# Optimization experiments

Measured on AMD Instinct MI355X. Metric: run time of the kernel, lower is better.

Reference implementation:

```python
import jax, jax.numpy as jnp
import numpy as np

EPS = 1e-6
DECAY = 0.9   # spike_decay
THR = 0.5     # spike_threshold
SBETA = 10.0  # surrogate beta
KW = 4        # depthwise short-conv kernel width (causal)


def _rms(x, w):
    return x * jax.lax.rsqrt(jnp.mean(x * x, axis=-1, keepdims=True) + EPS) * w


def setup_inputs() -> dict:
    B, T, D, H, dk, dv, r, dff = 2, 2048, 1024, 8, 64, 64, 64, 4096
    keys = iter(jax.random.split(jax.random.key(0), 24))
    def g(shape, s=0.02):
        return jax.random.normal(next(keys), shape, jnp.float32) * s
    return {
        'x': jax.random.normal(next(keys), (B, T, D), jnp.float32),
        'norm_in_w': jnp.ones((D,), jnp.float32),
        'conv_w': g((D, 1, KW), 0.3),
        'conv_b': jnp.zeros((D,), jnp.float32),
        'Wq': g((D, H * dk)),
        'Wk': g((D, H * dk)),
        'Wv': g((D, H * dv)),
        'Wo': g((H * dv, D)),
        'Wspike': g((D, H * dk), 0.1),  # larger init so LIF actually spikes
        'Wau': g((D, r)),
        'bau': jnp.zeros((r,), jnp.float32),
        'Wad': g((r, H * dk)),
        'bad': jnp.zeros((H * dk,), jnp.float32),
        'alpha_spike': jnp.zeros((1, H, dk), jnp.float32),
        'Wbeta': g((D, H)),
        'bbeta': jnp.zeros((H,), jnp.float32),
        'beta_spike': jnp.zeros((1, H, dk), jnp.float32),
        'head_norm_w': jnp.ones((H, dv), jnp.float32),
        'Wu1': g((D, r)),
        'bu1': jnp.zeros((r,), jnp.float32),
        'Wu2': g((r, D)),
        'bu2': jnp.zeros((D,), jnp.float32),
        'ff_norm_w': jnp.ones((D,), jnp.float32),
        'Wff1': g((D, dff)),
        'Wff3': g((D, dff)),
        'Wff2': g((dff, D)),
    }


def reference(x, norm_in_w, conv_w, conv_b, Wq, Wk, Wv, Wo, Wspike,
              Wau, bau, Wad, bad, alpha_spike, Wbeta, bbeta, beta_spike,
              head_norm_w, Wu1, bu1, Wu2, bu2, ff_norm_w, Wff1, Wff3, Wff2):
    B, T, D = x.shape
    H, dk = alpha_spike.shape[1], alpha_spike.shape[2]
    dv = head_norm_w.shape[1]

    # --- input norm + causal depthwise short conv + SiLU ---
    h = _rms(x, norm_in_w)
    hc = jnp.transpose(h, (0, 2, 1))                         # [B,D,T]
    conv = jax.lax.conv_general_dilated(
        hc, conv_w, window_strides=(1,), padding=[(KW - 1, 0)],
        dimension_numbers=('NCH', 'OIH', 'NCH'), feature_group_count=D)
    conv = conv + conv_b[None, :, None]
    h = jax.nn.silu(jnp.transpose(conv, (0, 2, 1)))          # [B,T,D]

    def heads(z, d):
        return z.reshape(B, T, H, d)

    q = heads(h @ Wq, dk)
    k = heads(h @ Wk, dk)
    v = heads(h @ Wv, dv)
    q = q / (jnp.linalg.norm(q, axis=-1, keepdims=True) + 1e-6)
    k = k / (jnp.linalg.norm(k, axis=-1, keepdims=True) + 1e-6)
    drive = heads(h @ Wspike, dk)                            # LIF drive [B,T,H,dk]
    alpha_base = heads(jax.nn.silu(h @ Wau + bau) @ Wad + bad, dk)
    beta_base = h @ Wbeta + bbeta                            # [B,T,H]

    asp = alpha_spike[0]                                     # [H,dk]
    bsp = beta_spike[0]                                      # [H,dk]

    def step(carry, ins):
        s, mem = carry                                       # s [B,H,dk,dv], mem [B,H,dk]
        qt, kt, vt, dt, at, bt = ins
        # LIF with surrogate-gradient spike (straight-through), soft reset
        mem = DECAY * mem + dt
        sg = jax.nn.sigmoid(SBETA * (mem - THR))
        hard = (mem > THR).astype(mem.dtype)
        spike = sg + jax.lax.stop_gradient(hard - sg)
        mem = mem - spike * THR
        # spiking-modulated gates
        alpha = jax.nn.sigmoid(at + asp * spike)             # [B,H,dk]
        beta = jax.nn.sigmoid(bt[..., None] + jnp.sum(spike * bsp, -1, keepdims=True))  # [B,H,1]
        active = (jnp.sum(jnp.abs(spike), -1, keepdims=True) > 0).astype(qt.dtype)      # [B,H,1]
        alpha = jnp.where(active > 0, alpha, jnp.ones_like(alpha))
        beta = beta * active
        # gated delta-rule fast-weight update
        s = s * alpha[..., None]
        pred = jnp.einsum('bhk,bhkv->bhv', kt, s)
        s = s + (beta * kt)[..., None] * (vt - pred)[:, :, None, :]
        out = jnp.einsum('bhk,bhkv->bhv', qt, s)
        return (s, mem), out

    s0 = jnp.zeros((B, H, dk, dv), x.dtype)
    m0 = jnp.zeros((B, H, dk), x.dtype)
    xs = (jnp.moveaxis(q, 1, 0), jnp.moveaxis(k, 1, 0), jnp.moveaxis(v, 1, 0),
          jnp.moveaxis(drive, 1, 0), jnp.moveaxis(alpha_base, 1, 0),
          jnp.moveaxis(beta_base, 1, 0))
    _, y = jax.lax.scan(step, (s0, m0), xs)                  # [T,B,H,dv]
    y = jnp.moveaxis(y, 0, 1)                                # [B,T,H,dv]

    # headwise RMS norm, merge heads
    y = y * jax.lax.rsqrt(jnp.mean(y * y, axis=-1, keepdims=True) + EPS) * head_norm_w
    y = y.reshape(B, T, H * dv)

    # gated output projection + residual
    gate = jax.nn.sigmoid(jax.nn.silu(x @ Wu1 + bu1) @ Wu2 + bu2)
    y = x + (y @ Wo) * gate

    # SwiGLU FFN + residual
    z = _rms(y, ff_norm_w)
    y = y + (jax.nn.silu(z @ Wff1) * (z @ Wff3)) @ Wff2
    return y
```

## Files before the change

### kernel.cpp

```cpp
#include <hip/hip_runtime.h>
#include <hip/hip_bf16.h>

#define BB 2
#define TT 2048
#define DD 1024
#define HH 8
#define HKk 512
#define BTt 4096
#define CC 16
#define NT 128
#define PREPSZ 4608

typedef unsigned short u16;
typedef __attribute__((ext_vector_type(8))) short bf16x8;
typedef __attribute__((ext_vector_type(4))) float f32x4;

__device__ __forceinline__ u16 f2bf(float v) {
  union { float f; unsigned u; } c; c.f = v;
  return (u16)((c.u + 0x7fffu + ((c.u >> 16) & 1u)) >> 16);
}
__device__ __forceinline__ float bf2f(u16 v) {
  union { unsigned u; float f; } c; c.u = ((unsigned)v) << 16; return c.f;
}
__device__ __forceinline__ float sigm(float x) { return 1.f / (1.f + expf(-x)); }

template <int CTRL>
__device__ __forceinline__ float dppx(float x) {
  union { float f; int i; } c; c.f = x;
  c.i = __builtin_amdgcn_update_dpp(c.i, c.i, CTRL, 0xf, 0xf, false);
  return c.f;
}

__device__ __forceinline__ void gld16(const u16* g, u16* l) {
  __builtin_amdgcn_global_load_lds((const __attribute__((address_space(1))) void*)g,
                                   (__attribute__((address_space(3))) void*)l, 16, 0, 0);
}

struct TransJobs {
  const float* src[8];
  u16* dst[8];
  int K[8], N[8], rs[8], ro[8], lognx[8];
  int off[8];
};
__global__ __launch_bounds__(256) void ktransB(TransJobs J) {
  __shared__ u16 t[32][33];
  int bid = blockIdx.x;
  int j = 0;
#pragma unroll
  for (int q = 1; q < 8; q++) j += (bid >= J.off[q]) ? 1 : 0;
  int local = bid - J.off[j];
  const float* src = J.src[j];
  u16* dst = J.dst[j];
  int K = J.K[j], N = J.N[j], rs = J.rs[j], ro = J.ro[j];
  int nxm = (1 << J.lognx[j]) - 1;
  int n0 = (local & nxm) * 32, k0 = (local >> J.lognx[j]) * 32;
  int tx = threadIdx.x & 31, ty0 = threadIdx.x >> 5;
#pragma unroll
  for (int i = 0; i < 32; i += 8)
    t[ty0 + i][tx] = f2bf(src[(size_t)(k0 + ty0 + i) * N + n0 + tx]);
  __syncthreads();
#pragma unroll
  for (int i = 0; i < 32; i += 8)
    dst[((size_t)(n0 + ty0 + i) * rs + ro) * K + k0 + tx] = t[tx][ty0 + i];
}

__global__ __launch_bounds__(256) void krms(const float* __restrict__ x,
                                            const float* __restrict__ w,
                                            void* __restrict__ out, int obf) {
  size_t row = blockIdx.x;
  __shared__ float red[4];
  float vals[4];
  float s = 0.f;
#pragma unroll
  for (int i = 0; i < 4; i++) {
    vals[i] = x[row * DD + threadIdx.x + i * 256];
    s += vals[i] * vals[i];
  }
#pragma unroll
  for (int off = 32; off; off >>= 1) s += __shfl_xor(s, off);
  if ((threadIdx.x & 63) == 0) red[threadIdx.x >> 6] = s;
  __syncthreads();
  float tot = red[0] + red[1] + red[2] + red[3];
  float sc = rsqrtf(tot * (1.f / DD) + 1e-6f);
#pragma unroll
  for (int i = 0; i < 4; i++) {
    size_t idx = row * DD + threadIdx.x + i * 256;
    float vv = vals[i] * sc * w[threadIdx.x + i * 256];
    if (obf) ((u16*)out)[idx] = f2bf(vv);
    else ((float*)out)[idx] = vv;
  }
}

__global__ __launch_bounds__(256) void kconv(const float* __restrict__ hin,
                                             const float* __restrict__ cw,
                                             const float* __restrict__ cb,
                                             u16* __restrict__ hout) {
  size_t i = (size_t)blockIdx.x * 256 + threadIdx.x;
  int d = (int)(i & 1023);
  int bt = (int)(i >> 10);
  int b = bt >> 11, t = bt & 2047;
  float acc = cb[d];
#pragma unroll
  for (int j = 0; j < 4; j++) {
    int tt = t - 3 + j;
    if (tt >= 0) acc += hin[(((size_t)(b * TT + tt)) << 10) + d] * cw[d * 4 + j];
  }
  hout[i] = f2bf(acc * sigm(acc));
}

__global__ __launch_bounds__(256) void kgemm(const void* __restrict__ A, int abf,
                                             const float* __restrict__ Bm,
                                             const float* __restrict__ bias,
                                             float* __restrict__ C,
                                             int M, int N, int K, int act) {
  __shared__ __align__(16) float As[16][64];
  __shared__ __align__(16) float Bs[16][64];
  int tid = threadIdx.x;
  int tx = tid & 15, ty = tid >> 4;
  int row0 = blockIdx.y * 64, col0 = blockIdx.x * 64;
  float acc[4][4] = {};
  for (int k0 = 0; k0 < K; k0 += 16) {
#pragma unroll
    for (int l = 0; l < 4; l++) {
      int e = tid * 4 + l;
      int m = e >> 4, kk = e & 15;
      int gr = row0 + m;
      size_t ai = (size_t)gr * K + k0 + kk;
      As[kk][m] = (gr < M) ? (abf ? bf2f(((const u16*)A)[ai]) : ((const float*)A)[ai]) : 0.f;
    }
#pragma unroll
    for (int l = 0; l < 4; l++) {
      int e = tid + l * 256;
      int kk = e >> 6, n = e & 63;
      int gc = col0 + n;
      Bs[kk][n] = (gc < N) ? Bm[(size_t)(k0 + kk) * N + gc] : 0.f;
    }
    __syncthreads();
#pragma unroll
    for (int kk = 0; kk < 16; kk++) {
      float4 av = *(const float4*)&As[kk][ty * 4];
      float4 bv = *(const float4*)&Bs[kk][tx * 4];
      float a[4] = {av.x, av.y, av.z, av.w};
      float b[4] = {bv.x, bv.y, bv.z, bv.w};
#pragma unroll
      for (int i = 0; i < 4; i++)
#pragma unroll
        for (int j = 0; j < 4; j++) acc[i][j] += a[i] * b[j];
    }
    __syncthreads();
  }
#pragma unroll
  for (int i = 0; i < 4; i++) {
    int r = row0 + ty * 4 + i;
    if (r >= M) continue;
#pragma unroll
    for (int j = 0; j < 4; j++) {
      int cc = col0 + tx * 4 + j;
      if (cc >= N) continue;
      float vv = acc[i][j];
      if (bias) vv += bias[cc];
      if (act == 1) vv = vv * sigm(vv);
      else if (act == 2) vv = sigm(vv);
      C[(size_t)r * N + cc] = vv;
    }
  }
}

struct SJobs {
  const void* A[3];
  const float* B[3];
  const float* bias[3];
  float* C[3];
  int N[3], act[3], abf[3];
};
__global__ __launch_bounds__(256) void kgemmS3(SJobs J) {
  __shared__ __align__(16) float As[32][17];
  __shared__ __align__(16) float Bs[32][64];
  int job = blockIdx.x >> 8;
  int row0 = (blockIdx.x & 255) << 4;
  const void* A = J.A[job];
  const float* Bm = J.B[job];
  int N = J.N[job], abf = J.abf[job], act = J.act[job];
  int tid = threadIdx.x;
  int tx = tid & 63;
  int ty = tid >> 6;
  float acc[4] = {};
  for (int k0 = 0; k0 < DD; k0 += 32) {
    __syncthreads();
#pragma unroll
    for (int l = 0; l < 2; l++) {
      int idx = tid * 2 + l;
      int k = idx & 31, m = idx >> 5;
      size_t ai = (size_t)(row0 + m) * DD + k0 + k;
      As[k][m] = abf ? bf2f(((const u16*)A)[ai]) : ((const float*)A)[ai];
    }
#pragma unroll
    for (int l = 0; l < 8; l++) {
      int idx = tid + l * 256;
      int n = idx & 63, k = idx >> 6;
      Bs[k][n] = (n < N) ? Bm[(size_t)(k0 + k) * N + n] : 0.f;
    }
    __syncthreads();
#pragma unroll
    for (int kk = 0; kk < 32; kk++) {
      float b = Bs[kk][tx];
#pragma unroll
      for (int i = 0; i < 4; i++) acc[i] += As[kk][ty * 4 + i] * b;
    }
  }
  if (tx < N) {
    float* C = J.C[job];
    const float* bias = J.bias[job];
#pragma unroll
    for (int i = 0; i < 4; i++) {
      float vv = acc[i] + bias[tx];
      if (act == 1) vv = vv * sigm(vv);
      C[(size_t)(row0 + ty * 4 + i) * N + tx] = vv;
    }
  }
}

template <int EPI>
__global__ __launch_bounds__(256) void kmfma(
    const u16* __restrict__ A, int lda, const u16* __restrict__ Bt,
    void* __restrict__ C, int ldc, int M, int N, int K,
    const float* __restrict__ g1f, const float* __restrict__ g2f,
    const float* __restrict__ f1) {
  __shared__ __align__(16) u16 As[128 * 64];
  __shared__ __align__(16) u16 Bs[128 * 64];
  int tid = threadIdx.x;
  int lane = tid & 63, wv = tid >> 6;
  int m0 = (wv & 1) * 64, n0 = (wv >> 1) * 64;
  int ml = lane & 15, kq = (lane >> 4) << 3;
  int nbx = gridDim.x;
  int flat = blockIdx.y * nbx + blockIdx.x;
  int nwg = nbx * gridDim.y;
  int work = (flat & 7) * (nwg >> 3) + (flat >> 3);
  int row0 = (work / nbx) * 128, col0 = (work % nbx) * 128;
  int lrow = lane >> 3;
  int lslot = (lane & 7) ^ lrow;

  f32x4 acc[4][4];
#pragma unroll
  for (int i = 0; i < 4; i++)
#pragma unroll
    for (int j = 0; j < 4; j++) acc[i][j] = (f32x4){0.f, 0.f, 0.f, 0.f};

  for (int k0 = 0; k0 < K; k0 += 64) {
    __syncthreads();
#pragma unroll
    for (int j = 0; j < 4; j++) {
      int r0 = j * 32 + wv * 8;
      gld16(&A[(size_t)(row0 + r0 + lrow) * lda + k0 + lslot * 8], &As[r0 * 64]);
      gld16(&Bt[(size_t)(col0 + r0 + lrow) * K + k0 + lslot * 8], &Bs[r0 * 64]);
    }
    __syncthreads();
#pragma unroll
    for (int kk = 0; kk < 64; kk += 32) {
      int sw = (((kk + kq) >> 3) ^ (ml & 7)) << 3;
      bf16x8 af[4], bfr[4];
#pragma unroll
      for (int i = 0; i < 4; i++)
        af[i] = *(const bf16x8*)&As[(m0 + i * 16 + ml) * 64 + sw];
#pragma unroll
      for (int j = 0; j < 4; j++)
        bfr[j] = *(const bf16x8*)&Bs[(n0 + j * 16 + ml) * 64 + sw];
#pragma unroll
      for (int i = 0; i < 4; i++)
#pragma unroll
        for (int j = 0; j < 4; j++)
          acc[i][j] = __builtin_amdgcn_mfma_f32_16x16x32_bf16(af[i], bfr[j], acc[i][j], 0, 0, 0);
    }
  }
  int rbase = row0 + m0 + ((lane >> 4) << 2);
  if (EPI == 4) {
    int donorm = (col0 + n0) < 1024;
#pragma unroll
    for (int i = 0; i < 4; i++) {
#pragma unroll
      for (int r = 0; r < 4; r++) {
        float s = 0.f;
#pragma unroll
        for (int j = 0; j < 4; j++) { float v = acc[i][j][r]; s += v * v; }
#pragma unroll
        for (int off = 1; off < 16; off <<= 1) s += __shfl_xor(s, off);
        float sc = donorm ? 1.f / (sqrtf(s) + 1e-6f) : 1.f;
        int gr = rbase + i * 16 + r;
#pragma unroll
        for (int j = 0; j < 4; j++) {
          int gc = col0 + n0 + j * 16 + ml;
          ((float*)C)[(size_t)gr * ldc + gc] = acc[i][j][r] * sc;
        }
      }
    }
    return;
  }
#pragma unroll
  for (int i = 0; i < 4; i++) {
#pragma unroll
    for (int j = 0; j < 4; j++) {
      int gc = col0 + n0 + j * 16 + ml;
#pragma unroll
      for (int r = 0; r < 4; r++) {
        int gr = rbase + i * 16 + r;
        float v = acc[i][j][r];
        if (EPI == 0) {
          ((float*)C)[(size_t)gr * ldc + gc] = v;
        } else if (EPI == 1) {
          float p = __shfl_xor(v, 1);
          float a0 = (lane & 1) ? p : v;
          float b0 = (lane & 1) ? v : p;
          float g = a0 * sigm(a0) * b0;
          if (!(lane & 1))
            ((u16*)C)[(size_t)gr * ldc + (gc >> 1)] = f2bf(g);
        } else if (EPI == 2) {
          size_t idx = (size_t)gr * ldc + gc;
          ((float*)C)[idx] = g1f[idx] + v * g2f[idx];
        } else {
          size_t idx = (size_t)gr * ldc + gc;
          ((float*)C)[idx] = f1[idx] + v;
        }
      }
    }
  }
}

__global__ __launch_bounds__(256) void kheadnorm(const float* __restrict__ y,
                                                 const float* __restrict__ hw,
                                                 u16* __restrict__ yo) {
  int lane = threadIdx.x & 63;
  size_t r = (size_t)blockIdx.x * 4 + (threadIdx.x >> 6);
  int h = (int)(r & 7);
  float vv = y[r * 64 + lane];
  float s = vv * vv;
#pragma unroll
  for (int off = 32; off; off >>= 1) s += __shfl_xor(s, off);
  yo[r * 64 + lane] = f2bf(vv * rsqrtf(s * (1.f / 64.f) + 1e-6f) * hw[h * 64 + lane]);
}

__global__ __launch_bounds__(64) void klifA(const float* __restrict__ dr, int drs,
                                            unsigned* __restrict__ masks) {
  int bh = blockIdx.x;
  int b = bh >> 3, h = bh & 7;
  int lane = threadIdx.x;
  float cur[32], nxt[32];
#pragma unroll
  for (int i = 0; i < 32; i++)
    cur[i] = dr[(size_t)(b * TT + i) * drs + h * 64 + lane];
  float mem = 0.f;
  for (int t0 = 0; t0 < TT; t0 += 32) {
    if (t0 + 32 < TT) {
#pragma unroll
      for (int i = 0; i < 32; i++)
        nxt[i] = dr[(size_t)(b * TT + t0 + 32 + i) * drs + h * 64 + lane];
    }
    unsigned m = 0;
#pragma unroll
    for (int i = 0; i < 32; i++) {
      mem = 0.9f * mem + cur[i];
      int s = (mem > 0.5f) ? 1 : 0;
      mem -= s ? 0.5f : 0.f;
      m |= ((unsigned)s) << i;
    }
    masks[((size_t)bh * 64 + (t0 >> 5)) * 64 + lane] = m;
#pragma unroll
    for (int i = 0; i < 32; i++) cur[i] = nxt[i];
  }
}

__global__ __launch_bounds__(64) void kprep(const float* __restrict__ X1,
                                            const float* __restrict__ ab,
                                            const float* __restrict__ bb,
                                            const float* __restrict__ asp,
                                            const float* __restrict__ bsp,
                                            const unsigned* __restrict__ masks,
                                            float* __restrict__ prep) {
  int blk = blockIdx.x;
  int bh = blk >> 7, T = blk & 127;
  int b = bh >> 3, h = bh & 7;
  int lane = threadIdx.x;
  size_t row0 = (size_t)(b * TT) + (size_t)T * CC;
  float* out = prep + (size_t)blk * PREPSZ;
  __shared__ float sKP[CC][68], sKiP[CC][68], sQP[CC][68];
  __shared__ float sBC[CC * CC], sG[CC * CC], sW[CC * CC], sBeta[CC];

  float aspk = asp[h * 64 + lane];
  float bspk = bsp[h * 64 + lane];
  float Pt[CC], kv[CC], kh[CC], bet[CC];
  {
    float P = 1.f;
#pragma unroll
    for (int t = 0; t < CC; t++) {
      size_t rt = row0 + t;
      int tg = T * CC + t;
      unsigned mw = masks[((size_t)bh * 64 + (tg >> 5)) * 64 + lane];
      int s = (mw >> (tg & 31)) & 1;
      unsigned long long act = __ballot(s != 0);
      float sp = (float)s;
      float abv = ab[rt * HKk + h * 64 + lane];
      int active = (act != 0ull);
      float a = active ? sigm(abv + aspk * sp) : 1.f;
      float r2 = sp * bspk;
#pragma unroll
      for (int off = 32; off; off >>= 1) r2 += __shfl_xor(r2, off);
      float bbv = bb[rt * HH + h];
      bet[t] = active ? sigm(bbv + r2) : 0.f;
      kv[t] = X1[rt * 2048 + h * 64 + 512 + lane];
      float qv = X1[rt * 2048 + h * 64 + lane];
      P *= a;
      Pt[t] = P;
      float qp = qv * P;
      sQP[t][lane] = qp;
      out[1024 + t * 64 + lane] = qp;
    }
    float PC = Pt[CC - 1];
#pragma unroll
    for (int t = 0; t < CC; t++) {
      float KiPv = kv[t] / Pt[t];
      sKP[t][lane] = kv[t] * Pt[t];
      sKiP[t][lane] = KiPv;
      kh[t] = PC * KiPv;
    }
    out[4096 + lane] = PC;
  }
  if (lane == 0) {
#pragma unroll
    for (int t = 0; t < CC; t++) sBeta[t] = bet[t];
  }
  __syncthreads();
#pragma unroll
  for (int t = 0; t < CC; t++) out[t * 64 + lane] = bet[t] * kv[t] * Pt[t];

#pragma unroll
  for (int i = 0; i < 4; i++) {
    int p = lane + 64 * i;
    int t2 = p >> 4, s2 = p & 15;
    float ac = 0.f, ag = 0.f;
#pragma unroll
    for (int k = 0; k < 64; k++) {
      float kip = sKiP[s2][k];
      ac += sKP[t2][k] * kip;
      ag += sQP[t2][k] * kip;
    }
    sBC[p] = (t2 > s2) ? sBeta[t2] * ac : 0.f;
    sG[p] = (t2 >= s2) ? ag : 0.f;
    sW[p] = 0.f;
  }
  __syncthreads();
  if (lane < CC) sW[lane * CC + lane] = 1.f;
  __syncthreads();

  for (int t = 1; t < CC; t++) {
    if (lane < t) {
      float a = -sBC[t * CC + lane];
      for (int s = lane + 1; s < t; s++) a -= sBC[t * CC + s] * sW[s * CC + lane];
      sW[t * CC + lane] = a;
    }
    __syncthreads();
  }
#pragma unroll
  for (int i = 0; i < 4; i++) {
    int p = lane + 64 * i;
    int t2 = p >> 4, s2 = p & 15;
    float gw = 0.f;
    if (s2 <= t2)
      for (int m = s2; m <= t2; m++) gw += sG[t2 * CC + m] * sW[m * CC + s2];
    out[4160 + p] = gw;
  }
#pragma unroll
  for (int r = 0; r < CC; r++) {
    float acc = 0.f;
    for (int s = r; s < CC; s++) acc += kh[s] * sW[s * CC + r];
    out[2048 + r * 64 + lane] = acc;
  }
#pragma unroll
  for (int t = 0; t < CC; t++)
    out[3072 + t * 64 + lane] = bet[t] * X1[(row0 + t) * 2048 + h * 64 + 1024 + lane];
}

__global__ __launch_bounds__(64, 1) void kscan2(const float* __restrict__ prep,
                                                float* __restrict__ y) {
  int bid = blockIdx.x;
  int bh = bid & 15, vg = bid >> 4;
  int b = bh >> 3, h = bh & 7;
  int lane = threadIdx.x;
  int kp = lane & 15, vv = lane >> 4;
  const float* base = prep + (size_t)bh * NT * PREPSZ;

  float4 S = make_float4(0.f, 0.f, 0.f, 0.f);
  float4 k1A[16], q1A[16], k1B[16], q1B[16];
#pragma unroll
  for (int t = 0; t < CC; t++) {
    k1A[t] = *(const float4*)(base + t * 64 + kp * 4);
    q1A[t] = *(const float4*)(base + 1024 + t * 64 + kp * 4);
  }
  size_t yb = (size_t)(b * TT) * HKk + h * 64 + vg * 4 + vv;

#define TILEBODY(TI, K1, Q1, K1N, Q1N)                                          \
  do {                                                                          \
    const float* bp = base + (size_t)(TI)*PREPSZ;                               \
    int TN = ((TI) + 1 < NT) ? (TI) + 1 : NT - 1;                               \
    const float* np = base + (size_t)TN * PREPSZ;                               \
         \
    float4 kh2[16], gw[4], a15;                                                 \
    float bvs;                                                                  \
    _Pragma("unroll") for (int r = 0; r < CC; r++)                              \
        kh2[r] = *(const float4*)(bp + 2048 + r * 64 + kp * 4);                 \
    a15 = *(const float4*)(bp + 4096 + kp * 4);                                 \
    _Pragma("unroll") for (int i = 0; i < 4; i++)                               \
        gw[i] = *(const float4*)(bp + 4160 + kp * 16 + i * 4);                  \
    bvs = bp[3072 + kp * 64 + vg * 4 + vv];                                     \
                                \
    float bt[16], qb[16];                                                       \
    _Pragma("unroll") for (int t = 0; t < CC; t++) {                            \
      bt[t] = K1[t].x * S.x + K1[t].y * S.y + K1[t].z * S.z + K1[t].w * S.w;    \
      qb[t] = Q1[t].x * S.x + Q1[t].y * S.y + Q1[t].z * S.z + Q1[t].w * S.w;    \
    }                                                                           \
                                                \
    _Pragma("unroll") for (int t = 0; t < CC; t++) {                            \
      K1N[t] = *(const float4*)(np + t * 64 + kp * 4);                          \
      Q1N[t] = *(const float4*)(np + 1024 + t * 64 + kp * 4);                   \
    }                                                                           \
           \
    float b8[8], b4[4], b2[2], bS;                                              \
    _Pragma("unroll") for (int j = 0; j < 8; j++) {                             \
      float snd = (kp & 8) ? bt[j] : bt[j + 8];                                 \
      float rcv = dppx<0x128>(snd);                                             \
      b8[j] = ((kp & 8) ? bt[j + 8] : bt[j]) + rcv;                             \
    }                                                                           \
    _Pragma("unroll") for (int j = 0; j < 4; j++) {                             \
      float snd = (kp & 4) ? b8[j] : b8[j + 4];                                 \
      float rcv = dppx<0x141>(snd);                                             \
      b4[j] = ((kp & 4) ? b8[j + 4] : b8[j]) + rcv;                             \
    }                                                                           \
    _Pragma("unroll") for (int j = 0; j < 2; j++) {                             \
      float snd = (kp & 2) ? b4[j] : b4[j + 2];                                 \
      float rcv = dppx<0x4E>(snd);                                              \
      b2[j] = ((kp & 2) ? b4[j + 2] : b4[j]) + rcv;                             \
    }                                                                           \
    {                                                                           \
      float snd = (kp & 1) ? b2[0] : b2[1];                                     \
      float rcv = dppx<0xB1>(snd);                                              \
      bS = ((kp & 1) ? b2[1] : b2[0]) + rcv;                                    \
    }                                                                           \
    float uS = bvs - bS;                                                        \
          \
    float u[16];                                                                \
    {                                                                           \
      float g = dppx<0xB1>(uS);                                                 \
      float a0 = (kp & 1) ? g : uS, a1 = (kp & 1) ? uS : g;                     \
      float g0 = dppx<0x4E>(a0), g1 = dppx<0x4E>(a1);                           \
      float c0 = (kp & 2) ? g0 : a0, c1 = (kp & 2) ? g1 : a1;                   \
      float c2 = (kp & 2) ? a0 : g0, c3 = (kp & 2) ? a1 : g1;                   \
      float h0 = dppx<0x141>(c0), h1 = dppx<0x141>(c1);                         \
      float h2 = dppx<0x141>(c2), h3 = dppx<0x141>(c3);                         \
      float d0 = (kp & 4) ? h0 : c0, d1 = (kp & 4) ? h1 : c1;                   \
      float d2 = (kp & 4) ? h2 : c2, d3 = (kp & 4) ? h3 : c3;                   \
      float d4 = (kp & 4) ? c0 : h0, d5 = (kp & 4) ? c1 : h1;                   \
      float d6 = (kp & 4) ? c2 : h2, d7 = (kp & 4) ? c3 : h3;                   \
      float e0 = dppx<0x128>(d0), e1 = dppx<0x128>(d1);                         \
      float e2 = dppx<0x128>(d2), e3 = dppx<0x128>(d3);                         \
      float e4 = dppx<0x128>(d4), e5 = dppx<0x128>(d5);                         \
      float e6 = dppx<0x128>(d6), e7 = dppx<0x128>(d7);                         \
      u[0] = (kp & 8) ? e0 : d0; u[1] = (kp & 8) ? e1 : d1;                     \
      u[2] = (kp & 8) ? e2 : d2; u[3] = (kp & 8) ? e3 : d3;                     \
      u[4] = (kp & 8) ? e4 : d4; u[5] = (kp & 8) ? e5 : d5;                     \
      u[6] = (kp & 8) ? e6 : d6; u[7] = (kp & 8) ? e7 : d7;                     \
      u[8] = (kp & 8) ? d0 : e0; u[9] = (kp & 8) ? d1 : e1;                     \
      u[10] = (kp & 8) ? d2 : e2; u[11] = (kp & 8) ? d3 : e3;                   \
      u[12] = (kp & 8) ? d4 : e4; u[13] = (kp & 8) ? d5 : e5;                   \
      u[14] = (kp & 8) ? d6 : e6; u[15] = (kp & 8) ? d7 : e7;                   \
    }                                                                           \
                             \
    float p8[8], p4[4], p2[2], qsel;                                            \
    _Pragma("unroll") for (int j = 0; j < 8; j++) {                             \
      float snd = (kp & 8) ? qb[j] : qb[j + 8];                                 \
      float rcv = dppx<0x128>(snd);                                             \
      p8[j] = ((kp & 8) ? qb[j + 8] : qb[j]) + rcv;                             \
    }                                                                           \
    _Pragma("unroll") for (int j = 0; j < 4; j++) {                             \
      float snd = (kp & 4) ? p8[j] : p8[j + 4];                                 \
      float rcv = dppx<0x141>(snd);                                             \
      p4[j] = ((kp & 4) ? p8[j + 4] : p8[j]) + rcv;                             \
    }                                                                           \
    _Pragma("unroll") for (int j = 0; j < 2; j++) {                             \
      float snd = (kp & 2) ? p4[j] : p4[j + 2];                                 \
      float rcv = dppx<0x4E>(snd);                                              \
      p2[j] = ((kp & 2) ? p4[j + 2] : p4[j]) + rcv;                             \
    }                                                                           \
    {                                                                           \
      float snd = (kp & 1) ? p2[0] : p2[1];                                     \
      float rcv = dppx<0xB1>(snd);                                              \
      qsel = ((kp & 1) ? p2[1] : p2[0]) + rcv;                                  \
    }                                                                           \
                    \
    float o = qsel;                                                             \
    _Pragma("unroll") for (int i = 0; i < 4; i++)                               \
        o += gw[i].x * u[i * 4] + gw[i].y * u[i * 4 + 1] +                      \
             gw[i].z * u[i * 4 + 2] + gw[i].w * u[i * 4 + 3];                   \
    y[yb + (size_t)((TI)*CC + kp) * HKk] = o;                                   \
                          \
    S.x *= a15.x; S.y *= a15.y; S.z *= a15.z; S.w *= a15.w;                     \
    _Pragma("unroll") for (int r = 0; r < CC; r++) {                            \
      S.x += kh2[r].x * u[r]; S.y += kh2[r].y * u[r];                           \
      S.z += kh2[r].z * u[r]; S.w += kh2[r].w * u[r];                           \
    }                                                                           \
  } while (0)

  for (int T = 0; T < NT; T += 2) {
    TILEBODY(T, k1A, q1A, k1B, q1B);
    TILEBODY(T + 1, k1B, q1B, k1A, q1A);
  }
#undef TILEBODY
}

extern "C" void kernel_launch(void* const* d_in, const int* in_sizes, int n_in,
                              void* d_out, int out_size, void* d_ws, size_t ws_size,
                              hipStream_t stream) {
  const float *x = (const float*)d_in[0], *norm_in_w = (const float*)d_in[1],
              *conv_w = (const float*)d_in[2], *conv_b = (const float*)d_in[3],
              *Wq = (const float*)d_in[4], *Wk = (const float*)d_in[5],
              *Wv = (const float*)d_in[6], *Wo = (const float*)d_in[7],
              *Wspike = (const float*)d_in[8], *Wau = (const float*)d_in[9],
              *bau = (const float*)d_in[10], *Wad = (const float*)d_in[11],
              *bad_ = (const float*)d_in[12], *asp = (const float*)d_in[13],
              *Wbeta = (const float*)d_in[14], *bbeta = (const float*)d_in[15],
              *bsp = (const float*)d_in[16], *hnw = (const float*)d_in[17],
              *Wu1 = (const float*)d_in[18], *bu1 = (const float*)d_in[19],
              *Wu2 = (const float*)d_in[20], *bu2 = (const float*)d_in[21],
              *ffw = (const float*)d_in[22], *Wff1 = (const float*)d_in[23],
              *Wff3 = (const float*)d_in[24], *Wff2 = (const float*)d_in[25];
  (void)in_sizes; (void)n_in; (void)out_size; (void)ws_size;

  char* wsb = (char*)d_ws;
  size_t off = 0;
  auto alloc = [&](size_t bytes) {
    void* p = wsb + off;
    off += (bytes + 255) & ~(size_t)255;
    return p;
  };
  float* h    = (float*)alloc((size_t)BTt * DD * 4);
  u16*   hc   = (u16*)alloc((size_t)BTt * DD * 2);
  size_t qoff = off;
  float* X1   = (float*)alloc((size_t)BTt * 2048 * 4);
  float* ab   = (float*)alloc((size_t)BTt * HKk * 4);
  float* au   = (float*)alloc((size_t)BTt * 64 * 4);
  float* bb   = (float*)alloc((size_t)BTt * HH * 4);
  float* u1   = (float*)alloc((size_t)BTt * 64 * 4);
  float* gate = (float*)alloc((size_t)BTt * DD * 4);
  float* yat  = (float*)alloc((size_t)BTt * HKk * 4);
  u16* yat_bf = (u16*)alloc((size_t)BTt * HKk * 2);
  u16* f_bf   = (u16*)(wsb + qoff);
  float* y2   = (float*)alloc((size_t)BTt * DD * 4);
  u16* z_bf   = (u16*)alloc((size_t)BTt * DD * 2);
  u16* WtX    = (u16*)alloc((size_t)2048 * 1024 * 2);
  u16* WtO    = (u16*)alloc((size_t)1024 * 512 * 2);
  u16* WtFF   = (u16*)alloc((size_t)8192 * 1024 * 2);
  u16* WtF2   = (u16*)alloc((size_t)1024 * 4096 * 2);
  float* prep = (float*)alloc((size_t)16 * NT * PREPSZ * 4);
  unsigned* masks = (unsigned*)alloc((size_t)16 * 64 * 64 * 4);

  {
    TransJobs J;
    J.src[0] = Wq;     J.dst[0] = WtX + (size_t)0 * 512 * 1024; J.K[0] = 1024; J.N[0] = 512;  J.rs[0] = 1; J.ro[0] = 0; J.lognx[0] = 4;
    J.src[1] = Wk;     J.dst[1] = WtX + (size_t)1 * 512 * 1024; J.K[1] = 1024; J.N[1] = 512;  J.rs[1] = 1; J.ro[1] = 0; J.lognx[1] = 4;
    J.src[2] = Wv;     J.dst[2] = WtX + (size_t)2 * 512 * 1024; J.K[2] = 1024; J.N[2] = 512;  J.rs[2] = 1; J.ro[2] = 0; J.lognx[2] = 4;
    J.src[3] = Wspike; J.dst[3] = WtX + (size_t)3 * 512 * 1024; J.K[3] = 1024; J.N[3] = 512;  J.rs[3] = 1; J.ro[3] = 0; J.lognx[3] = 4;
    J.src[4] = Wo;     J.dst[4] = WtO;                          J.K[4] = 512;  J.N[4] = 1024; J.rs[4] = 1; J.ro[4] = 0; J.lognx[4] = 5;
    J.src[5] = Wff1;   J.dst[5] = WtFF;                         J.K[5] = 1024; J.N[5] = 4096; J.rs[5] = 2; J.ro[5] = 0; J.lognx[5] = 7;
    J.src[6] = Wff3;   J.dst[6] = WtFF;                         J.K[6] = 1024; J.N[6] = 4096; J.rs[6] = 2; J.ro[6] = 1; J.lognx[6] = 7;
    J.src[7] = Wff2;   J.dst[7] = WtF2;                         J.K[7] = 4096; J.N[7] = 1024; J.rs[7] = 1; J.ro[7] = 0; J.lognx[7] = 5;
    J.off[0] = 0;    J.off[1] = 512;  J.off[2] = 1024; J.off[3] = 1536;
    J.off[4] = 2048; J.off[5] = 2560; J.off[6] = 6656; J.off[7] = 10752;
    ktransB<<<14848, 256, 0, stream>>>(J);
  }

  krms<<<BTt, 256, 0, stream>>>(x, norm_in_w, h, 0);
  kconv<<<BTt * DD / 256, 256, 0, stream>>>(h, conv_w, conv_b, hc);

  kmfma<4><<<dim3(16, 32), 256, 0, stream>>>(
      hc, 1024, WtX, X1, 2048, BTt, 2048, 1024, nullptr, nullptr, nullptr);

  {
    SJobs S;
    S.A[0] = hc; S.B[0] = Wau;   S.bias[0] = bau;   S.C[0] = au; S.N[0] = 64; S.act[0] = 1; S.abf[0] = 1;
    S.A[1] = hc; S.B[1] = Wbeta; S.bias[1] = bbeta; S.C[1] = bb; S.N[1] = 8;  S.act[1] = 0; S.abf[1] = 1;
    S.A[2] = x;  S.B[2] = Wu1;   S.bias[2] = bu1;   S.C[2] = u1; S.N[2] = 64; S.act[2] = 1; S.abf[2] = 0;
    kgemmS3<<<768, 256, 0, stream>>>(S);
  }
  kgemm<<<dim3(8, 64), 256, 0, stream>>>(au, 0, Wad, bad_, ab, BTt, HKk, 64, 0);

  klifA<<<BB * HH, 64, 0, stream>>>(X1 + 1536, 2048, masks);
  kprep<<<16 * NT, 64, 0, stream>>>(X1, ab, bb, asp, bsp, masks, prep);
  kscan2<<<16 * 16, 64, 0, stream>>>(prep, yat);
  kheadnorm<<<BTt * HH / 4, 256, 0, stream>>>(yat, hnw, yat_bf);

  kgemm<<<dim3(16, 64), 256, 0, stream>>>(u1, 0, Wu2, bu2, gate, BTt, DD, 64, 2);

  kmfma<2><<<dim3(8, 32), 256, 0, stream>>>(
      yat_bf, 512, WtO, y2, 1024, BTt, 1024, 512, x, gate, nullptr);

  krms<<<BTt, 256, 0, stream>>>(y2, ffw, z_bf, 1);
  kmfma<1><<<dim3(64, 32), 256, 0, stream>>>(
      z_bf, 1024, WtFF, f_bf, 4096, BTt, 8192, 1024, nullptr, nullptr, nullptr);
  kmfma<3><<<dim3(8, 32), 256, 0, stream>>>(
      f_bf, 4096, WtF2, d_out, 1024, BTt, 1024, 4096, nullptr, nullptr, y2);
}
```

Baseline: 803.1 us.

## Split scan key dimension across half-waves to double scan block count

The chunked delta-rule scan now has each lane hold two key-dimension entries of the state instead of four. The key dimension is split across the two half-waves, and their partial dot products are combined with a cross-half shuffle. This doubles the grid from 256 to 512 single-wave blocks, each covering 2 value columns instead of 4, which exposes more parallelism on the long serial scan and lightens per-lane register pressure. In exchange, every tile adds shuffles, half the lanes do redundant output work, and the prep data is read twice as many times overall.

```diff
diff --git a/kernel.cpp b/kernel.cpp
--- a/kernel.cpp
+++ b/kernel.cpp
@@ -484,44 +484,49 @@
   int bh = bid & 15, vg = bid >> 4;
   int b = bh >> 3, h = bh & 7;
   int lane = threadIdx.x;
-  int kp = lane & 15, vv = lane >> 4;
+  int kp = lane & 15;
+  int vv = lane >> 4;
+  int kh = vv >> 1;
+  int cl = vv & 1;
+  int kbase = kh * 32 + kp * 2;
   const float* base = prep + (size_t)bh * NT * PREPSZ;
 
-  float4 S = make_float4(0.f, 0.f, 0.f, 0.f);
-  float4 k1A[16], q1A[16], k1B[16], q1B[16];
+  float2 S = make_float2(0.f, 0.f);
+  float2 k1A[16], q1A[16], k1B[16], q1B[16];
 #pragma unroll
   for (int t = 0; t < CC; t++) {
-    k1A[t] = *(const float4*)(base + t * 64 + kp * 4);
-    q1A[t] = *(const float4*)(base + 1024 + t * 64 + kp * 4);
-  }
-  size_t yb = (size_t)(b * TT) * HKk + h * 64 + vg * 4 + vv;
+    k1A[t] = *(const float2*)(base + t * 64 + kbase);
+    q1A[t] = *(const float2*)(base + 1024 + t * 64 + kbase);
+  }
+  size_t yb = (size_t)(b * TT) * HKk + h * 64 + vg * 2 + cl;
 
 #define TILEBODY(TI, K1, Q1, K1N, Q1N)                                          \
   do {                                                                          \
     const float* bp = base + (size_t)(TI)*PREPSZ;                               \
     int TN = ((TI) + 1 < NT) ? (TI) + 1 : NT - 1;                               \
     const float* np = base + (size_t)TN * PREPSZ;                               \
-         \
-    float4 kh2[16], gw[4], a15;                                                 \
+                                      \
+    float2 kh2[16], a15;                                                        \
+    float4 gwa, gwb;                                                            \
     float bvs;                                                                  \
+    bvs = bp[3072 + kp * 64 + vg * 2 + cl];                                     \
+    gwa = *(const float4*)(bp + 4160 + kp * 16);                                \
+    gwb = *(const float4*)(bp + 4160 + kp * 16 + 4);                            \
+    a15 = *(const float2*)(bp + 4096 + kbase);                                  \
     _Pragma("unroll") for (int r = 0; r < CC; r++)                              \
-        kh2[r] = *(const float4*)(bp + 2048 + r * 64 + kp * 4);                 \
-    a15 = *(const float4*)(bp + 4096 + kp * 4);                                 \
-    _Pragma("unroll") for (int i = 0; i < 4; i++)                               \
-        gw[i] = *(const float4*)(bp + 4160 + kp * 16 + i * 4);                  \
-    bvs = bp[3072 + kp * 64 + vg * 4 + vv];                                     \
-                                \
+        kh2[r] = *(const float2*)(bp + 2048 + r * 64 + kbase);                  \
+                                 \
     float bt[16], qb[16];                                                       \
     _Pragma("unroll") for (int t = 0; t < CC; t++) {                            \
-      bt[t] = K1[t].x * S.x + K1[t].y * S.y + K1[t].z * S.z + K1[t].w * S.w;    \
-      qb[t] = Q1[t].x * S.x + Q1[t].y * S.y + Q1[t].z * S.z + Q1[t].w * S.w;    \
+      bt[t] = K1[t].x * S.x + K1[t].y * S.y;                                    \
+      qb[t] = Q1[t].x * S.x + Q1[t].y * S.y;                                    \
     }                                                                           \
                                                 \
     _Pragma("unroll") for (int t = 0; t < CC; t++) {                            \
-      K1N[t] = *(const float4*)(np + t * 64 + kp * 4);                          \
-      Q1N[t] = *(const float4*)(np + 1024 + t * 64 + kp * 4);                   \
-    }                                                                           \
-           \
+      K1N[t] = *(const float2*)(np + t * 64 + kbase);                           \
+      Q1N[t] = *(const float2*)(np + 1024 + t * 64 + kbase);                    \
+    }                                                                           \
+         \
     float b8[8], b4[4], b2[2], bS;                                              \
     _Pragma("unroll") for (int j = 0; j < 8; j++) {                             \
       float snd = (kp & 8) ? bt[j] : bt[j + 8];                                 \
@@ -543,8 +548,9 @@
       float rcv = dppx<0xB1>(snd);                                              \
       bS = ((kp & 1) ? b2[1] : b2[0]) + rcv;                                    \
     }                                                                           \
+    bS += __shfl_xor(bS, 32);       \
     float uS = bvs - bS;                                                        \
-          \
+           \
     float u[16];                                                                \
     {                                                                           \
       float g = dppx<0xB1>(uS);                                                 \
@@ -571,7 +577,7 @@
       u[12] = (kp & 8) ? d4 : e4; u[13] = (kp & 8) ? d5 : e5;                   \
       u[14] = (kp & 8) ? d6 : e6; u[15] = (kp & 8) ? d7 : e7;                   \
     }                                                                           \
-                             \
+                 \
     float p8[8], p4[4], p2[2], qsel;                                            \
     _Pragma("unroll") for (int j = 0; j < 8; j++) {                             \
       float snd = (kp & 8) ? qb[j] : qb[j + 8];                                 \
@@ -593,17 +599,20 @@
       float rcv = dppx<0xB1>(snd);                                              \
       qsel = ((kp & 1) ? p2[1] : p2[0]) + rcv;                                  \
     }                                                                           \
-                    \
-    float o = qsel;                                                             \
-    _Pragma("unroll") for (int i = 0; i < 4; i++)                               \
-        o += gw[i].x * u[i * 4] + gw[i].y * u[i * 4 + 1] +                      \
-             gw[i].z * u[i * 4 + 2] + gw[i].w * u[i * 4 + 3];                   \
-    y[yb + (size_t)((TI)*CC + kp) * HKk] = o;                                   \
+    qsel += __shfl_xor(qsel, 32);                                               \
+               \
+    float o = qsel + gwa.x * u[0] + gwa.y * u[1] + gwa.z * u[2] +               \
+              gwa.w * u[3] + gwb.x * u[4] + gwb.y * u[5] + gwb.z * u[6] +       \
+              gwb.w * u[7];                                                     \
+    o += bp[4160 + kp * 16 + 8] * u[8] + bp[4160 + kp * 16 + 9] * u[9] +        \
+         bp[4160 + kp * 16 + 10] * u[10] + bp[4160 + kp * 16 + 11] * u[11] +    \
+         bp[4160 + kp * 16 + 12] * u[12] + bp[4160 + kp * 16 + 13] * u[13] +    \
+         bp[4160 + kp * 16 + 14] * u[14] + bp[4160 + kp * 16 + 15] * u[15];     \
+    if (vv < 2) y[yb + (size_t)((TI)*CC + kp) * HKk] = o;                       \
                           \
-    S.x *= a15.x; S.y *= a15.y; S.z *= a15.z; S.w *= a15.w;                     \
+    S.x *= a15.x; S.y *= a15.y;                                                 \
     _Pragma("unroll") for (int r = 0; r < CC; r++) {                            \
       S.x += kh2[r].x * u[r]; S.y += kh2[r].y * u[r];                           \
-      S.z += kh2[r].z * u[r]; S.w += kh2[r].w * u[r];                           \
     }                                                                           \
   } while (0)
 
@@ -692,7 +701,7 @@
 
   klifA<<<BB * HH, 64, 0, stream>>>(X1 + 1536, 2048, masks);
   kprep<<<16 * NT, 64, 0, stream>>>(X1, ab, bb, asp, bsp, masks, prep);
-  kscan2<<<16 * 16, 64, 0, stream>>>(prep, yat);
+  kscan2<<<16 * 32, 64, 0, stream>>>(prep, yat);
   kheadnorm<<<BTt * HH / 4, 256, 0, stream>>>(yat, hnw, yat_bf);
 
   kgemm<<<dim3(16, 64), 256, 0, stream>>>(u1, 0, Wu2, bu2, gate, BTt, DD, 64, 2);
```

Result: slower. 923.7 us (+15.0%).

## Stage scan k/q tiles through double-buffered LDS instead of register prefetch

Applied to the files above, without the earlier changes.

The chunked delta-rule scan kernel used to prefetch the next tile's k and q rows into 128 float4 registers per lane, with redundant loads across the four value groups. It now loads each tile with coalesced float4 reads (4 per lane), writes them to a double-buffered shared-memory array, and prefetches two tiles ahead in registers. This cuts VGPR pressure and duplicate global traffic, at the cost of LDS reads inside the serial loop and a single-wavefront LDS dependency without explicit barriers.

```diff
diff --git a/kernel.cpp b/kernel.cpp
--- a/kernel.cpp
+++ b/kernel.cpp
@@ -486,132 +486,152 @@
   int lane = threadIdx.x;
   int kp = lane & 15, vv = lane >> 4;
   const float* base = prep + (size_t)bh * NT * PREPSZ;
+  __shared__ __align__(16) float lbuf[2][2048];
 
   float4 S = make_float4(0.f, 0.f, 0.f, 0.f);
-  float4 k1A[16], q1A[16], k1B[16], q1B[16];
-#pragma unroll
-  for (int t = 0; t < CC; t++) {
-    k1A[t] = *(const float4*)(base + t * 64 + kp * 4);
-    q1A[t] = *(const float4*)(base + 1024 + t * 64 + kp * 4);
+  float4 gk[4], gq[4];
+#pragma unroll
+  for (int r = 0; r < 4; r++) {
+    gk[r] = *(const float4*)(base + r * 256 + lane * 4);
+    gq[r] = *(const float4*)(base + 1024 + r * 256 + lane * 4);
+  }
+#pragma unroll
+  for (int r = 0; r < 4; r++) {
+    *(float4*)&lbuf[0][r * 256 + lane * 4] = gk[r];
+    *(float4*)&lbuf[0][1024 + r * 256 + lane * 4] = gq[r];
+  }
+#pragma unroll
+  for (int r = 0; r < 4; r++) {
+    gk[r] = *(const float4*)(base + PREPSZ + r * 256 + lane * 4);
+    gq[r] = *(const float4*)(base + PREPSZ + 1024 + r * 256 + lane * 4);
   }
   size_t yb = (size_t)(b * TT) * HKk + h * 64 + vg * 4 + vv;
 
-#define TILEBODY(TI, K1, Q1, K1N, Q1N)                                          \
-  do {                                                                          \
-    const float* bp = base + (size_t)(TI)*PREPSZ;                               \
-    int TN = ((TI) + 1 < NT) ? (TI) + 1 : NT - 1;                               \
-    const float* np = base + (size_t)TN * PREPSZ;                               \
-         \
-    float4 kh2[16], gw[4], a15;                                                 \
-    float bvs;                                                                  \
-    _Pragma("unroll") for (int r = 0; r < CC; r++)                              \
-        kh2[r] = *(const float4*)(bp + 2048 + r * 64 + kp * 4);                 \
-    a15 = *(const float4*)(bp + 4096 + kp * 4);                                 \
-    _Pragma("unroll") for (int i = 0; i < 4; i++)                               \
-        gw[i] = *(const float4*)(bp + 4160 + kp * 16 + i * 4);                  \
-    bvs = bp[3072 + kp * 64 + vg * 4 + vv];                                     \
-                                \
-    float bt[16], qb[16];                                                       \
-    _Pragma("unroll") for (int t = 0; t < CC; t++) {                            \
-      bt[t] = K1[t].x * S.x + K1[t].y * S.y + K1[t].z * S.z + K1[t].w * S.w;    \
-      qb[t] = Q1[t].x * S.x + Q1[t].y * S.y + Q1[t].z * S.z + Q1[t].w * S.w;    \
-    }                                                                           \
-                                                \
-    _Pragma("unroll") for (int t = 0; t < CC; t++) {                            \
-      K1N[t] = *(const float4*)(np + t * 64 + kp * 4);                          \
-      Q1N[t] = *(const float4*)(np + 1024 + t * 64 + kp * 4);                   \
-    }                                                                           \
-           \
-    float b8[8], b4[4], b2[2], bS;                                              \
-    _Pragma("unroll") for (int j = 0; j < 8; j++) {                             \
-      float snd = (kp & 8) ? bt[j] : bt[j + 8];                                 \
-      float rcv = dppx<0x128>(snd);                                             \
-      b8[j] = ((kp & 8) ? bt[j + 8] : bt[j]) + rcv;                             \
-    }                                                                           \
-    _Pragma("unroll") for (int j = 0; j < 4; j++) {                             \
-      float snd = (kp & 4) ? b8[j] : b8[j + 4];                                 \
-      float rcv = dppx<0x141>(snd);                                             \
-      b4[j] = ((kp & 4) ? b8[j + 4] : b8[j]) + rcv;                             \
-    }                                                                           \
-    _Pragma("unroll") for (int j = 0; j < 2; j++) {                             \
-      float snd = (kp & 2) ? b4[j] : b4[j + 2];                                 \
-      float rcv = dppx<0x4E>(snd);                                              \
-      b2[j] = ((kp & 2) ? b4[j + 2] : b4[j]) + rcv;                             \
-    }                                                                           \
-    {                                                                           \
-      float snd = (kp & 1) ? b2[0] : b2[1];                                     \
-      float rcv = dppx<0xB1>(snd);                                              \
-      bS = ((kp & 1) ? b2[1] : b2[0]) + rcv;                                    \
-    }                                                                           \
-    float uS = bvs - bS;                                                        \
-          \
-    float u[16];                                                                \
-    {                                                                           \
-      float g = dppx<0xB1>(uS);                                                 \
-      float a0 = (kp & 1) ? g : uS, a1 = (kp & 1) ? uS : g;                     \
-      float g0 = dppx<0x4E>(a0), g1 = dppx<0x4E>(a1);                           \
-      float c0 = (kp & 2) ? g0 : a0, c1 = (kp & 2) ? g1 : a1;                   \
-      float c2 = (kp & 2) ? a0 : g0, c3 = (kp & 2) ? a1 : g1;                   \
-      float h0 = dppx<0x141>(c0), h1 = dppx<0x141>(c1);                         \
-      float h2 = dppx<0x141>(c2), h3 = dppx<0x141>(c3);                         \
-      float d0 = (kp & 4) ? h0 : c0, d1 = (kp & 4) ? h1 : c1;                   \
-      float d2 = (kp & 4) ? h2 : c2, d3 = (kp & 4) ? h3 : c3;                   \
-      float d4 = (kp & 4) ? c0 : h0, d5 = (kp & 4) ? c1 : h1;                   \
-      float d6 = (kp & 4) ? c2 : h2, d7 = (kp & 4) ? c3 : h3;                   \
-      float e0 = dppx<0x128>(d0), e1 = dppx<0x128>(d1);                         \
-      float e2 = dppx<0x128>(d2), e3 = dppx<0x128>(d3);                         \
-      float e4 = dppx<0x128>(d4), e5 = dppx<0x128>(d5);                         \
-      float e6 = dppx<0x128>(d6), e7 = dppx<0x128>(d7);                         \
-      u[0] = (kp & 8) ? e0 : d0; u[1] = (kp & 8) ? e1 : d1;                     \
-      u[2] = (kp & 8) ? e2 : d2; u[3] = (kp & 8) ? e3 : d3;                     \
-      u[4] = (kp & 8) ? e4 : d4; u[5] = (kp & 8) ? e5 : d5;                     \
-      u[6] = (kp & 8) ? e6 : d6; u[7] = (kp & 8) ? e7 : d7;                     \
-      u[8] = (kp & 8) ? d0 : e0; u[9] = (kp & 8) ? d1 : e1;                     \
-      u[10] = (kp & 8) ? d2 : e2; u[11] = (kp & 8) ? d3 : e3;                   \
-      u[12] = (kp & 8) ? d4 : e4; u[13] = (kp & 8) ? d5 : e5;                   \
-      u[14] = (kp & 8) ? d6 : e6; u[15] = (kp & 8) ? d7 : e7;                   \
-    }                                                                           \
-                             \
-    float p8[8], p4[4], p2[2], qsel;                                            \
-    _Pragma("unroll") for (int j = 0; j < 8; j++) {                             \
-      float snd = (kp & 8) ? qb[j] : qb[j + 8];                                 \
-      float rcv = dppx<0x128>(snd);                                             \
-      p8[j] = ((kp & 8) ? qb[j + 8] : qb[j]) + rcv;                             \
-    }                                                                           \
-    _Pragma("unroll") for (int j = 0; j < 4; j++) {                             \
-      float snd = (kp & 4) ? p8[j] : p8[j + 4];                                 \
-      float rcv = dppx<0x141>(snd);                                             \
-      p4[j] = ((kp & 4) ? p8[j + 4] : p8[j]) + rcv;                             \
-    }                                                                           \
-    _Pragma("unroll") for (int j = 0; j < 2; j++) {                             \
-      float snd = (kp & 2) ? p4[j] : p4[j + 2];                                 \
-      float rcv = dppx<0x4E>(snd);                                              \
-      p2[j] = ((kp & 2) ? p4[j + 2] : p4[j]) + rcv;                             \
-    }                                                                           \
-    {                                                                           \
-      float snd = (kp & 1) ? p2[0] : p2[1];                                     \
-      float rcv = dppx<0xB1>(snd);                                              \
-      qsel = ((kp & 1) ? p2[1] : p2[0]) + rcv;                                  \
-    }                                                                           \
-                    \
-    float o = qsel;                                                             \
-    _Pragma("unroll") for (int i = 0; i < 4; i++)                               \
-        o += gw[i].x * u[i * 4] + gw[i].y * u[i * 4 + 1] +                      \
-             gw[i].z * u[i * 4 + 2] + gw[i].w * u[i * 4 + 3];                   \
-    y[yb + (size_t)((TI)*CC + kp) * HKk] = o;                                   \
-                          \
-    S.x *= a15.x; S.y *= a15.y; S.z *= a15.z; S.w *= a15.w;                     \
-    _Pragma("unroll") for (int r = 0; r < CC; r++) {                            \
-      S.x += kh2[r].x * u[r]; S.y += kh2[r].y * u[r];                           \
-      S.z += kh2[r].z * u[r]; S.w += kh2[r].w * u[r];                           \
-    }                                                                           \
-  } while (0)
-
-  for (int T = 0; T < NT; T += 2) {
-    TILEBODY(T, k1A, q1A, k1B, q1B);
-    TILEBODY(T + 1, k1B, q1B, k1A, q1A);
-  }
-#undef TILEBODY
+  for (int T = 0; T < NT; T++) {
+    const float* bp = base + (size_t)T * PREPSZ;
+    const float* lb = lbuf[T & 1];
+    float4 kh2[16], gw[4], a15;
+    float bvs;
+    bvs = bp[3072 + kp * 64 + vg * 4 + vv];
+#pragma unroll
+    for (int i = 0; i < 4; i++)
+      gw[i] = *(const float4*)(bp + 4160 + kp * 16 + i * 4);
+    a15 = *(const float4*)(bp + 4096 + kp * 4);
+#pragma unroll
+    for (int r = 0; r < CC; r++)
+      kh2[r] = *(const float4*)(bp + 2048 + r * 64 + kp * 4);
+    float bt[16], qb[16];
+#pragma unroll
+    for (int t = 0; t < CC; t++) {
+      float4 kvv = *(const float4*)&lb[t * 64 + kp * 4];
+      float4 qvv = *(const float4*)&lb[1024 + t * 64 + kp * 4];
+      bt[t] = kvv.x * S.x + kvv.y * S.y + kvv.z * S.z + kvv.w * S.w;
+      qb[t] = qvv.x * S.x + qvv.y * S.y + qvv.z * S.z + qvv.w * S.w;
+    }
+    float b8[8], b4[4], b2[2], bS;
+#pragma unroll
+    for (int j = 0; j < 8; j++) {
+      float snd = (kp & 8) ? bt[j] : bt[j + 8];
+      float rcv = dppx<0x128>(snd);
+      b8[j] = ((kp & 8) ? bt[j + 8] : bt[j]) + rcv;
+    }
+#pragma unroll
+    for (int j = 0; j < 4; j++) {
+      float snd = (kp & 4) ? b8[j] : b8[j + 4];
+      float rcv = dppx<0x141>(snd);
+      b4[j] = ((kp & 4) ? b8[j + 4] : b8[j]) + rcv;
+    }
+#pragma unroll
+    for (int j = 0; j < 2; j++) {
+      float snd = (kp & 2) ? b4[j] : b4[j + 2];
+      float rcv = dppx<0x4E>(snd);
+      b2[j] = ((kp & 2) ? b4[j + 2] : b4[j]) + rcv;
+    }
+    {
+      float snd = (kp & 1) ? b2[0] : b2[1];
+      float rcv = dppx<0xB1>(snd);
+      bS = ((kp & 1) ? b2[1] : b2[0]) + rcv;
+    }
+    float uS = bvs - bS;
+    float u[16];
+    {
+      float g = dppx<0xB1>(uS);
+      float a0 = (kp & 1) ? g : uS, a1 = (kp & 1) ? uS : g;
+      float g0 = dppx<0x4E>(a0), g1 = dppx<0x4E>(a1);
+      float c0 = (kp & 2) ? g0 : a0, c1 = (kp & 2) ? g1 : a1;
+      float c2 = (kp & 2) ? a0 : g0, c3 = (kp & 2) ? a1 : g1;
+      float h0 = dppx<0x141>(c0), h1 = dppx<0x141>(c1);
+      float h2 = dppx<0x141>(c2), h3 = dppx<0x141>(c3);
+      float d0 = (kp & 4) ? h0 : c0, d1 = (kp & 4) ? h1 : c1;
+      float d2 = (kp & 4) ? h2 : c2, d3 = (kp & 4) ? h3 : c3;
+      float d4 = (kp & 4) ? c0 : h0, d5 = (kp & 4) ? c1 : h1;
+      float d6 = (kp & 4) ? c2 : h2, d7 = (kp & 4) ? c3 : h3;
+      float e0 = dppx<0x128>(d0), e1 = dppx<0x128>(d1);
+      float e2 = dppx<0x128>(d2), e3 = dppx<0x128>(d3);
+      float e4 = dppx<0x128>(d4), e5 = dppx<0x128>(d5);
+      float e6 = dppx<0x128>(d6), e7 = dppx<0x128>(d7);
+      u[0] = (kp & 8) ? e0 : d0; u[1] = (kp & 8) ? e1 : d1;
+      u[2] = (kp & 8) ? e2 : d2; u[3] = (kp & 8) ? e3 : d3;
+      u[4] = (kp & 8) ? e4 : d4; u[5] = (kp & 8) ? e5 : d5;
+      u[6] = (kp & 8) ? e6 : d6; u[7] = (kp & 8) ? e7 : d7;
+      u[8] = (kp & 8) ? d0 : e0; u[9] = (kp & 8) ? d1 : e1;
+      u[10] = (kp & 8) ? d2 : e2; u[11] = (kp & 8) ? d3 : e3;
+      u[12] = (kp & 8) ? d4 : e4; u[13] = (kp & 8) ? d5 : e5;
+      u[14] = (kp & 8) ? d6 : e6; u[15] = (kp & 8) ? d7 : e7;
+    }
+    float p8[8], p4[4], p2[2], qsel;
+#pragma unroll
+    for (int j = 0; j < 8; j++) {
+      float snd = (kp & 8) ? qb[j] : qb[j + 8];
+      float rcv = dppx<0x128>(snd);
+      p8[j] = ((kp & 8) ? qb[j + 8] : qb[j]) + rcv;
+    }
+#pragma unroll
+    for (int j = 0; j < 4; j++) {
+      float snd = (kp & 4) ? p8[j] : p8[j + 4];
+      float rcv = dppx<0x141>(snd);
+      p4[j] = ((kp & 4) ? p8[j + 4] : p8[j]) + rcv;
+    }
+#pragma unroll
+    for (int j = 0; j < 2; j++) {
+      float snd = (kp & 2) ? p4[j] : p4[j + 2];
+      float rcv = dppx<0x4E>(snd);
+      p2[j] = ((kp & 2) ? p4[j + 2] : p4[j]) + rcv;
+    }
+    {
+      float snd = (kp & 1) ? p2[0] : p2[1];
+      float rcv = dppx<0xB1>(snd);
+      qsel = ((kp & 1) ? p2[1] : p2[0]) + rcv;
+    }
+    float o = qsel;
+#pragma unroll
+    for (int i = 0; i < 4; i++)
+      o += gw[i].x * u[i * 4] + gw[i].y * u[i * 4 + 1] +
+           gw[i].z * u[i * 4 + 2] + gw[i].w * u[i * 4 + 3];
+    y[yb + (size_t)(T * CC + kp) * HKk] = o;
+    S.x *= a15.x; S.y *= a15.y; S.z *= a15.z; S.w *= a15.w;
+#pragma unroll
+    for (int r = 0; r < CC; r++) {
+      S.x += kh2[r].x * u[r]; S.y += kh2[r].y * u[r];
+      S.z += kh2[r].z * u[r]; S.w += kh2[r].w * u[r];
+    }
+    if (T < NT - 1) {
+      float* nb = lbuf[(T + 1) & 1];
+#pragma unroll
+      for (int r = 0; r < 4; r++) {
+        *(float4*)&nb[r * 256 + lane * 4] = gk[r];
+        *(float4*)&nb[1024 + r * 256 + lane * 4] = gq[r];
+      }
+      if (T + 2 < NT) {
+        const float* np2 = base + (size_t)(T + 2) * PREPSZ;
+#pragma unroll
+        for (int r = 0; r < 4; r++) {
+          gk[r] = *(const float4*)(np2 + r * 256 + lane * 4);
+          gq[r] = *(const float4*)(np2 + 1024 + r * 256 + lane * 4);
+        }
+      }
+    }
+  }
 }
 
 extern "C" void kernel_launch(void* const* d_in, const int* in_sizes, int n_in,
```

Result: slower. 965.3 us (+20.2%).
